# Kernel optimization log

Measured on AMD Instinct MI355X. Metric: run time of the kernel, lower is better.

Reference implementation:

```python
import jax, jax.numpy as jnp
import numpy as np
from jax import lax

KS = 3
PAD = 1
STRIDE = 1
N = KS * KS  # 9 sampling points
BN_EPS = 1e-5


def conv2d(x, w, stride=1, pad=0):
    return lax.conv_general_dilated(
        x, w, (stride, stride), [(pad, pad), (pad, pad)],
        dimension_numbers=('NCHW', 'OIHW', 'NCHW'))


def bn_inf(x, g, b, m, v):
    inv = g / jnp.sqrt(v + BN_EPS)
    return x * inv[None, :, None, None] + (b - m * inv)[None, :, None, None]


def gather_corners(x_flat, qx, qy, Wp):
    # x_flat: [B, C, Hp*Wp]; qx, qy: [B, H, W, N] int32
    B, C, _ = x_flat.shape
    idx = (qx * Wp + qy).reshape(B, 1, -1)
    out = jnp.take_along_axis(x_flat, jnp.broadcast_to(idx, (B, C, idx.shape[-1])), axis=-1)
    return out.reshape(B, C, *qx.shape[1:])  # [B, C, H, W, N]


def deform_conv_forward(x, w_conv1, g1, b1, m1, v1, w_dw, g2, b2, m2, v2,
                        w_conv2, g3, b3, m3, v3, w_out):
    B, C, H, W = x.shape
    identity = x

    # offset branch: Conv2d_BN(1x1) -> dwconv(3x3)+BN+ReLU -> Conv2d_BN(1x1)
    f = jax.nn.relu(bn_inf(conv2d(x, w_conv1), g1, b1, m1, v1))
    off = jax.nn.relu(bn_inf(conv2d(f, w_dw, pad=1), g2, b2, m2, v2))
    off = jax.nn.relu(bn_inf(conv2d(off, w_conv2), g3, b3, m3, v3))  # [B, 2N, H, W]
    off = off.transpose(0, 2, 3, 1)  # [B, H, W, 2N]

    # zero-pad input
    xp = jnp.pad(x, ((0, 0), (0, 0), (PAD, PAD), (PAD, PAD)))
    Hp, Wp = H + 2 * PAD, W + 2 * PAD

    # sampling locations p = p_0 + p_n + offset (x = row, y = col)
    rng = jnp.arange(-(KS - 1) // 2, (KS - 1) // 2 + 1, dtype=x.dtype)
    pnx, pny = jnp.meshgrid(rng, rng, indexing='ij')
    pnx, pny = pnx.ravel(), pny.ravel()  # [N]
    p0x = jnp.arange(1, H * STRIDE + 1, STRIDE, dtype=x.dtype)  # [H]
    p0y = jnp.arange(1, W * STRIDE + 1, STRIDE, dtype=x.dtype)  # [W]
    px = p0x[None, :, None, None] + pnx[None, None, None, :] + off[..., :N]  # [B,H,W,N]
    py = p0y[None, None, :, None] + pny[None, None, None, :] + off[..., N:]

    # integer corners (floor / floor+1, clamped) -- non-differentiable (detached in torch)
    flx = jnp.floor(lax.stop_gradient(px))
    fly = jnp.floor(lax.stop_gradient(py))
    qlt_x = jnp.clip(flx, 0, Hp - 1).astype(jnp.int32)
    qlt_y = jnp.clip(fly, 0, Wp - 1).astype(jnp.int32)
    qrb_x = jnp.clip(flx + 1, 0, Hp - 1).astype(jnp.int32)
    qrb_y = jnp.clip(fly + 1, 0, Wp - 1).astype(jnp.int32)

    # clamp continuous coords
    px = jnp.clip(px, 0, Hp - 1)
    py = jnp.clip(py, 0, Wp - 1)

    fx_lt = qlt_x.astype(px.dtype)
    fy_lt = qlt_y.astype(px.dtype)
    fx_rb = qrb_x.astype(px.dtype)
    fy_rb = qrb_y.astype(px.dtype)

    g_lt = (1 + (fx_lt - px)) * (1 + (fy_lt - py))
    g_rb = (1 - (fx_rb - px)) * (1 - (fy_rb - py))
    g_lb = (1 + (fx_lt - px)) * (1 - (fy_rb - py))
    g_rt = (1 - (fx_rb - px)) * (1 + (fy_lt - py))

    x_flat = xp.reshape(B, C, Hp * Wp)
    x_lt = gather_corners(x_flat, qlt_x, qlt_y, Wp)
    x_rb = gather_corners(x_flat, qrb_x, qrb_y, Wp)
    x_lb = gather_corners(x_flat, qlt_x, qrb_y, Wp)
    x_rt = gather_corners(x_flat, qrb_x, qlt_y, Wp)

    x_off = (g_lt[:, None] * x_lt + g_rb[:, None] * x_rb
             + g_lb[:, None] * x_lb + g_rt[:, None] * x_rt)  # [B,C,H,W,N]

    # reshape [B,C,H,W,ks,ks] -> [B,C,H*ks,W*ks] (matches torch _reshape_x_offset)
    x_off = x_off.reshape(B, C, H, W, KS, KS).transpose(0, 1, 2, 4, 3, 5)
    x_off = x_off.reshape(B, C, H * KS, W * KS)

    out = conv2d(x_off, w_out, stride=KS)  # [B, outc, H, W]
    return identity + out


def setup_inputs():
    key = jax.random.key(0)
    ks = jax.random.split(key, 8)
    B, C, H, W = 2, 64, 128, 128
    hid = int(C * 0.25)  # 16
    off_c = 2 * N  # 18
    x = jax.random.normal(ks[0], (B, C, H, W), jnp.float32)
    w_conv1 = jax.random.normal(ks[1], (hid, C, 1, 1), jnp.float32) * 0.1
    w_dw = jax.random.normal(ks[2], (off_c, hid, 3, 3), jnp.float32) * 0.05
    w_conv2 = jax.random.normal(ks[3], (off_c, off_c, 1, 1), jnp.float32) * 0.1
    w_out = jax.random.normal(ks[4], (C, C, KS, KS), jnp.float32) * 0.05

    def bn_params(k, c):
        k1, k2 = jax.random.split(k)
        return (1.0 + 0.1 * jax.random.normal(k1, (c,), jnp.float32),
                0.1 * jax.random.normal(k2, (c,), jnp.float32),
                jnp.zeros((c,), jnp.float32), jnp.ones((c,), jnp.float32))

    g1, b1, m1, v1 = bn_params(ks[5], hid)
    g2, b2, m2, v2 = bn_params(ks[6], off_c)
    g3, b3, m3, v3 = bn_params(ks[7], off_c)
    return dict(x=x, w_conv1=w_conv1, g1=g1, b1=b1, m1=m1, v1=v1,
                w_dw=w_dw, g2=g2, b2=b2, m2=m2, v2=v2,
                w_conv2=w_conv2, g3=g3, b3=b3, m3=m3, v3=v3, w_out=w_out)


def reference(x, w_conv1, g1, b1, m1, v1, w_dw, g2, b2, m2, v2,
              w_conv2, g3, b3, m3, v3, w_out):
    return deform_conv_forward(x, w_conv1, g1, b1, m1, v1, w_dw, g2, b2, m2, v2,
                               w_conv2, g3, b3, m3, v3, w_out)
```

## Files before the change

kernel.cpp:

```cpp
#include <hip/hip_runtime.h>

namespace {

constexpr int Hh = 128, Ww = 128, HW = 128 * 128;
constexpr int Cin = 64, HID = 16, OC = 18;

typedef __attribute__((ext_vector_type(8))) short short8;
typedef __attribute__((ext_vector_type(4))) float f32x4;

__device__ __forceinline__ unsigned short f2bf(float f) {
  unsigned u = __builtin_bit_cast(unsigned, f);
  unsigned rounded = u + 0x7fffu + ((u >> 16) & 1u);
  return (unsigned short)(rounded >> 16);
}
__device__ __forceinline__ float bf2f(unsigned short s) {
  unsigned u = ((unsigned)s) << 16;
  return __builtin_bit_cast(float, u);
}

__global__ __launch_bounds__(256) void k_pre(const float* __restrict__ x,
                                             unsigned short* __restrict__ xT,
                                             const float* __restrict__ w,
                                             unsigned short* __restrict__ wtb) {
  __shared__ float T[64][65];
  const int blk = blockIdx.x;
  const int t = threadIdx.x;
  if (blk >= 512) {
    const int i = (blk - 512) * 256 + t;
    const int oc = i / 576, r = i % 576;
    const int n = r >> 6, ic = r & 63;
    wtb[oc * 576 + r] = f2bf(w[oc * 576 + ic * 9 + n]);
    return;
  }
  const int b = blk >> 8;
  const int hw0 = (blk & 255) * 64;
  {
    const int p = t & 63, cg = t >> 6;
#pragma unroll
    for (int j = 0; j < 16; ++j) {
      const int c = cg * 16 + j;
      T[c][p] = x[(b * Cin + c) * HW + hw0 + p];
    }
  }
  __syncthreads();
  {
    const int c = t & 63, pg = t >> 6;
#pragma unroll
    for (int j = 0; j < 16; ++j) {
      const int p = pg * 16 + j;
      xT[((size_t)(b * HW + hw0 + p)) * 64 + c] = f2bf(T[c][p]);
    }
  }
}

__global__ __launch_bounds__(256) void k_off(
    const float* __restrict__ x, const float* __restrict__ w1,
    const float* __restrict__ g1, const float* __restrict__ b1,
    const float* __restrict__ m1, const float* __restrict__ v1,
    const float* __restrict__ wdw, const float* __restrict__ g2,
    const float* __restrict__ b2, const float* __restrict__ m2,
    const float* __restrict__ v2, const float* __restrict__ w2,
    const float* __restrict__ g3, const float* __restrict__ b3,
    const float* __restrict__ m3, const float* __restrict__ v3,
    float* __restrict__ offb) {
  __shared__ float fpart[2][HID][108];
  __shared__ float f[HID][108];
  __shared__ float off2[64][19];
  __shared__ float sA[16], bA[16], sB[18], bB[18], sC[18], bC[18];
  const int t = threadIdx.x;
  const int blk = blockIdx.x;
  const int b = blk >> 8;
  const int r0 = ((blk >> 3) & 31) * 4;
  const int c0 = (blk & 7) * 16;

  if (t >= 192 && t < 208) {
    int o = t - 192;
    float inv = g1[o] * rsqrtf(v1[o] + 1e-5f);
    sA[o] = inv; bA[o] = b1[o] - m1[o] * inv;
  } else if (t >= 208 && t < 226) {
    int o = t - 208;
    float inv = g2[o] * rsqrtf(v2[o] + 1e-5f);
    sB[o] = inv; bB[o] = b2[o] - m2[o] * inv;
  } else if (t >= 226 && t < 244) {
    int o = t - 226;
    float inv = g3[o] * rsqrtf(v3[o] + 1e-5f);
    sC[o] = inv; bC[o] = b3[o] - m3[o] * inv;
  }

  if (t < 216) {
    const int px = t % 108;
    const int cg = t / 108;
    const int hp = r0 + px / 18 - 1;
    const int wp = c0 + (px % 18) - 1;
    float acc[HID];
#pragma unroll
    for (int o = 0; o < HID; ++o) acc[o] = 0.f;
    if ((unsigned)hp < (unsigned)Hh && (unsigned)wp < (unsigned)Ww) {
      const float* xp = x + ((size_t)(b * Cin + cg * 32)) * HW + hp * Ww + wp;
      for (int c = 0; c < 32; ++c) {
        const float xv = xp[c * HW];
#pragma unroll
        for (int o = 0; o < HID; ++o)
          acc[o] = fmaf(w1[o * Cin + cg * 32 + c], xv, acc[o]);
      }
    }
#pragma unroll
    for (int o = 0; o < HID; ++o) fpart[cg][o][px] = acc[o];
  }
  __syncthreads();

  for (int idx = t; idx < 108 * HID; idx += 256) {
    const int px = idx % 108;
    const int o = idx / 108;
    const int hp = r0 + px / 18 - 1;
    const int wp = c0 + (px % 18) - 1;
    const float s = fpart[0][o][px] + fpart[1][o][px];
    const float y = fmaxf(fmaf(s, sA[o], bA[o]), 0.f);
    f[o][px] =
        ((unsigned)hp < (unsigned)Hh && (unsigned)wp < (unsigned)Ww) ? y : 0.f;
  }
  __syncthreads();

  if (t < 128) {
    const int ocg = t >> 6;
    const int px = t & 63;
    const int rr = px >> 4, cc = px & 15;
    float acc[9];
#pragma unroll
    for (int j = 0; j < 9; ++j) acc[j] = 0.f;
    for (int c = 0; c < HID; ++c) {
      float fv[9];
#pragma unroll
      for (int dh = 0; dh < 3; ++dh)
#pragma unroll
        for (int dw = 0; dw < 3; ++dw)
          fv[dh * 3 + dw] = f[c][(rr + dh) * 18 + cc + dw];
#pragma unroll
      for (int j = 0; j < 9; ++j) {
        const float* wj = wdw + (((ocg * 9 + j) * HID + c) * 9);
#pragma unroll
        for (int kk = 0; kk < 9; ++kk) acc[j] = fmaf(wj[kk], fv[kk], acc[j]);
      }
    }
#pragma unroll
    for (int j = 0; j < 9; ++j) {
      const int o = ocg * 9 + j;
      off2[px][o] = fmaxf(fmaf(acc[j], sB[o], bB[o]), 0.f);
    }
  }
  __syncthreads();

  if (t < 128) {
    const int ocg = t >> 6;
    const int px = t & 63;
    const int rr = px >> 4, cc = px & 15;
    float in[OC];
#pragma unroll
    for (int c = 0; c < OC; ++c) in[c] = off2[px][c];
    const int hw = (r0 + rr) * Ww + c0 + cc;
    float* dst = offb + ((size_t)(b * HW + hw)) * 18;
#pragma unroll
    for (int j = 0; j < 9; ++j) {
      const int o = ocg * 9 + j;
      float a = 0.f;
#pragma unroll
      for (int c = 0; c < OC; ++c) a = fmaf(w2[o * OC + c], in[c], a);
      dst[o] = fmaxf(fmaf(a, sC[o], bC[o]), 0.f);
    }
  }
}

__global__ __launch_bounds__(256) void k_main(
    const float* __restrict__ x, const unsigned short* __restrict__ xT,
    const float* __restrict__ offb, const unsigned short* __restrict__ wtb,
    float* __restrict__ out) {
  __shared__ unsigned short A[16][584];
  __shared__ float sg[16][9][4];
  __shared__ int si[16][9][4];
  const int blk = blockIdx.x;
  const int b = blk >> 10;
  const int t = threadIdx.x;
  const int hw0 = (blk & 1023) * 16;

  if (t < 144) {
    const int p = t / 9, n = t % 9;
    const int pix = blk * 16 + p;
    const int hw = pix & (HW - 1);
    const int h = hw >> 7, wc = hw & 127;
    const float offx = offb[pix * 18 + n];
    const float offy = offb[pix * 18 + 9 + n];
    const float px = (float)(h + (n / 3)) + offx;
    const float py = (float)(wc + (n % 3)) + offy;
    const float flx = floorf(px), fly = floorf(py);
    const float qltxf = fminf(fmaxf(flx, 0.f), 129.f);
    const float qltyf = fminf(fmaxf(fly, 0.f), 129.f);
    const float qrbxf = fminf(fmaxf(flx + 1.f, 0.f), 129.f);
    const float qrbyf = fminf(fmaxf(fly + 1.f, 0.f), 129.f);
    const float pxc = fminf(fmaxf(px, 0.f), 129.f);
    const float pyc = fminf(fmaxf(py, 0.f), 129.f);
    const float wx_lt = 1.f + (qltxf - pxc);
    const float wx_rb = 1.f - (qrbxf - pxc);
    const float wy_lt = 1.f + (qltyf - pyc);
    const float wy_rb = 1.f - (qrbyf - pyc);
    const int qltx = (int)qltxf, qlty = (int)qltyf;
    const int qrbx = (int)qrbxf, qrby = (int)qrbyf;
    const int cx[4] = {qltx, qrbx, qltx, qrbx};
    const int cy[4] = {qlty, qrby, qrby, qlty};
    const float gw[4] = {wx_lt * wy_lt, wx_rb * wy_rb, wx_lt * wy_rb,
                         wx_rb * wy_lt};
#pragma unroll
    for (int cc = 0; cc < 4; ++cc) {
      const bool valid =
          (cx[cc] >= 1) && (cx[cc] <= 128) && (cy[cc] >= 1) && (cy[cc] <= 128);
      si[p][n][cc] = valid ? ((cx[cc] - 1) * Ww + (cy[cc] - 1)) : 0;
      sg[p][n][cc] = valid ? gw[cc] : 0.f;
    }
  }
  __syncthreads();

  {
    const int p = t >> 4, ch4 = t & 15;
    const unsigned short* xb = xT + ((size_t)b * HW) * 64 + ch4 * 4;
#pragma unroll
    for (int n = 0; n < 9; ++n) {
      const ushort4 u0 = *(const ushort4*)(xb + (size_t)si[p][n][0] * 64);
      const ushort4 u1 = *(const ushort4*)(xb + (size_t)si[p][n][1] * 64);
      const ushort4 u2 = *(const ushort4*)(xb + (size_t)si[p][n][2] * 64);
      const ushort4 u3 = *(const ushort4*)(xb + (size_t)si[p][n][3] * 64);
      const float g0 = sg[p][n][0], g1 = sg[p][n][1], g2 = sg[p][n][2],
                  g3 = sg[p][n][3];
      float r0 = g0 * bf2f(u0.x);
      float r1 = g0 * bf2f(u0.y);
      float r2 = g0 * bf2f(u0.z);
      float r3 = g0 * bf2f(u0.w);
      r0 = fmaf(g1, bf2f(u1.x), r0); r1 = fmaf(g1, bf2f(u1.y), r1);
      r2 = fmaf(g1, bf2f(u1.z), r2); r3 = fmaf(g1, bf2f(u1.w), r3);
      r0 = fmaf(g2, bf2f(u2.x), r0); r1 = fmaf(g2, bf2f(u2.y), r1);
      r2 = fmaf(g2, bf2f(u2.z), r2); r3 = fmaf(g2, bf2f(u2.w), r3);
      r0 = fmaf(g3, bf2f(u3.x), r0); r1 = fmaf(g3, bf2f(u3.y), r1);
      r2 = fmaf(g3, bf2f(u3.z), r2); r3 = fmaf(g3, bf2f(u3.w), r3);
      ushort4 o;
      o.x = f2bf(r0); o.y = f2bf(r1); o.z = f2bf(r2); o.w = f2bf(r3);
      *(ushort4*)&A[p][n * 64 + ch4 * 4] = o;
    }
  }
  __syncthreads();

  {
    const int wv = t >> 6;
    const int lane = t & 63;
    const int l15 = lane & 15;
    const int quad = lane >> 4;
    const unsigned short* wrow = wtb + (size_t)(wv * 16 + l15) * 576 + quad * 8;
    const unsigned short* arow = &A[l15][quad * 8];
    f32x4 acc = {0.f, 0.f, 0.f, 0.f};
#pragma unroll
    for (int kb = 0; kb < 18; ++kb) {
      short8 af = *(const short8*)(wrow + kb * 32);
      short8 bf = *(const short8*)(arow + kb * 32);
      acc = __builtin_amdgcn_mfma_f32_16x16x32_bf16(af, bf, acc, 0, 0, 0);
    }
#pragma unroll
    for (int r = 0; r < 4; ++r) {
      const int oc = wv * 16 + quad * 4 + r;
      const size_t idx = ((size_t)(b * Cin + oc)) * HW + hw0 + l15;
      out[idx] = x[idx] + acc[r];
    }
  }
}

}

extern "C" void kernel_launch(void* const* d_in, const int* in_sizes, int n_in,
                              void* d_out, int out_size, void* d_ws,
                              size_t ws_size, hipStream_t stream) {
  const float* x = (const float*)d_in[0];
  const float* w1 = (const float*)d_in[1];
  const float* g1 = (const float*)d_in[2];
  const float* b1 = (const float*)d_in[3];
  const float* m1 = (const float*)d_in[4];
  const float* v1 = (const float*)d_in[5];
  const float* wdw = (const float*)d_in[6];
  const float* g2 = (const float*)d_in[7];
  const float* b2 = (const float*)d_in[8];
  const float* m2 = (const float*)d_in[9];
  const float* v2 = (const float*)d_in[10];
  const float* w2 = (const float*)d_in[11];
  const float* g3 = (const float*)d_in[12];
  const float* b3 = (const float*)d_in[13];
  const float* m3 = (const float*)d_in[14];
  const float* v3 = (const float*)d_in[15];
  const float* wout = (const float*)d_in[16];
  float* out = (float*)d_out;

  char* ws = (char*)d_ws;
  unsigned short* wtb = (unsigned short*)ws;
  unsigned short* xT = (unsigned short*)(ws + 81920);
  float* offb = (float*)(ws + 81920 + 4194304);

  k_pre<<<656, 256, 0, stream>>>(x, xT, wout, wtb);
  k_off<<<512, 256, 0, stream>>>(x, w1, g1, b1, m1, v1, wdw, g2, b2, m2, v2,
                                 w2, g3, b3, m3, v3, offb);
  k_main<<<2048, 256, 0, stream>>>(x, xT, offb, wtb, out);
}
```

Baseline: 153.2 us.

## Merge preprocessing and offset kernels into one launch with staged input halo

Combines the transpose/weight-conversion kernel and the offset-branch kernel into a single kernel, dispatching on block index, which removes one launch and lets the two independent jobs run concurrently. The offset branch now stages the 64-channel input halo tile into shared memory with a cooperative load before the 1x1 convolution, instead of each thread reading strided global memory. The union shared-memory buffer is larger (about 53 KB for every block), which may reduce occupancy for the transpose blocks.

```diff
diff --git a/kernel.cpp b/kernel.cpp
--- a/kernel.cpp
+++ b/kernel.cpp
@@ -18,60 +18,67 @@
   return __builtin_bit_cast(float, u);
 }
 
-__global__ __launch_bounds__(256) void k_pre(const float* __restrict__ x,
-                                             unsigned short* __restrict__ xT,
-                                             const float* __restrict__ w,
-                                             unsigned short* __restrict__ wtb) {
-  __shared__ float T[64][65];
+__global__ __launch_bounds__(256) void k_stage1(
+    const float* __restrict__ x, const float* __restrict__ wout,
+    const float* __restrict__ w1, const float* __restrict__ g1,
+    const float* __restrict__ b1, const float* __restrict__ m1,
+    const float* __restrict__ v1, const float* __restrict__ wdw,
+    const float* __restrict__ g2, const float* __restrict__ b2,
+    const float* __restrict__ m2, const float* __restrict__ v2,
+    const float* __restrict__ w2, const float* __restrict__ g3,
+    const float* __restrict__ b3, const float* __restrict__ m3,
+    const float* __restrict__ v3, unsigned short* __restrict__ xT,
+    unsigned short* __restrict__ wtb, float* __restrict__ offb) {
+  __shared__ __align__(16) char smem[53664];
   const int blk = blockIdx.x;
   const int t = threadIdx.x;
-  if (blk >= 512) {
+
+  if (blk < 512) {
+    float(*T)[65] = (float(*)[65])smem;
+    const int b = blk >> 8;
+    const int hw0 = (blk & 255) * 64;
+    {
+      const int p = t & 63, cg = t >> 6;
+#pragma unroll
+      for (int j = 0; j < 16; ++j) {
+        const int c = cg * 16 + j;
+        T[c][p] = x[(b * Cin + c) * HW + hw0 + p];
+      }
+    }
+    __syncthreads();
+    {
+      const int c = t & 63, pg = t >> 6;
+#pragma unroll
+      for (int j = 0; j < 16; ++j) {
+        const int p = pg * 16 + j;
+        xT[((size_t)(b * HW + hw0 + p)) * 64 + c] = f2bf(T[c][p]);
+      }
+    }
+    return;
+  }
+  if (blk < 656) {
     const int i = (blk - 512) * 256 + t;
     const int oc = i / 576, r = i % 576;
     const int n = r >> 6, ic = r & 63;
-    wtb[oc * 576 + r] = f2bf(w[oc * 576 + ic * 9 + n]);
+    wtb[oc * 576 + r] = f2bf(wout[oc * 576 + ic * 9 + n]);
     return;
   }
-  const int b = blk >> 8;
-  const int hw0 = (blk & 255) * 64;
-  {
-    const int p = t & 63, cg = t >> 6;
-#pragma unroll
-    for (int j = 0; j < 16; ++j) {
-      const int c = cg * 16 + j;
-      T[c][p] = x[(b * Cin + c) * HW + hw0 + p];
-    }
-  }
-  __syncthreads();
-  {
-    const int c = t & 63, pg = t >> 6;
-#pragma unroll
-    for (int j = 0; j < 16; ++j) {
-      const int p = pg * 16 + j;
-      xT[((size_t)(b * HW + hw0 + p)) * 64 + c] = f2bf(T[c][p]);
-    }
-  }
-}
-
-__global__ __launch_bounds__(256) void k_off(
-    const float* __restrict__ x, const float* __restrict__ w1,
-    const float* __restrict__ g1, const float* __restrict__ b1,
-    const float* __restrict__ m1, const float* __restrict__ v1,
-    const float* __restrict__ wdw, const float* __restrict__ g2,
-    const float* __restrict__ b2, const float* __restrict__ m2,
-    const float* __restrict__ v2, const float* __restrict__ w2,
-    const float* __restrict__ g3, const float* __restrict__ b3,
-    const float* __restrict__ m3, const float* __restrict__ v3,
-    float* __restrict__ offb) {
-  __shared__ float fpart[2][HID][108];
-  __shared__ float f[HID][108];
-  __shared__ float off2[64][19];
-  __shared__ float sA[16], bA[16], sB[18], bB[18], sC[18], bC[18];
-  const int t = threadIdx.x;
-  const int blk = blockIdx.x;
-  const int b = blk >> 8;
-  const int r0 = ((blk >> 3) & 31) * 4;
-  const int c0 = (blk & 7) * 16;
+
+  const int blk2 = blk - 656;
+  const int b = blk2 >> 8;
+  const int r0 = ((blk2 >> 3) & 31) * 4;
+  const int c0 = (blk2 & 7) * 16;
+  float* xh = (float*)smem;
+  float(*fpart)[HID][108] = (float(*)[HID][108])(smem + 27648);
+  float(*f)[108] = (float(*)[108])(smem + 41472);
+  float(*off2)[19] = (float(*)[19])(smem + 48384);
+  float* cst = (float*)(smem + 53248);
+  float* sA = cst;
+  float* bA = cst + 16;
+  float* sB = cst + 32;
+  float* bB = cst + 50;
+  float* sC = cst + 68;
+  float* bC = cst + 86;
 
   if (t >= 192 && t < 208) {
     int o = t - 192;
@@ -87,22 +94,31 @@
     sC[o] = inv; bC[o] = b3[o] - m3[o] * inv;
   }
 
+  {
+    const int base = b * Cin * HW;
+    for (int i = t; i < 64 * 108; i += 256) {
+      const int c = i / 108, px = i % 108;
+      const int hp = r0 + px / 18 - 1;
+      const int wp = c0 + (px % 18) - 1;
+      float v = 0.f;
+      if ((unsigned)hp < (unsigned)Hh && (unsigned)wp < (unsigned)Ww)
+        v = x[base + c * HW + hp * Ww + wp];
+      xh[c * 108 + px] = v;
+    }
+  }
+  __syncthreads();
+
   if (t < 216) {
     const int px = t % 108;
     const int cg = t / 108;
-    const int hp = r0 + px / 18 - 1;
-    const int wp = c0 + (px % 18) - 1;
     float acc[HID];
 #pragma unroll
     for (int o = 0; o < HID; ++o) acc[o] = 0.f;
-    if ((unsigned)hp < (unsigned)Hh && (unsigned)wp < (unsigned)Ww) {
-      const float* xp = x + ((size_t)(b * Cin + cg * 32)) * HW + hp * Ww + wp;
-      for (int c = 0; c < 32; ++c) {
-        const float xv = xp[c * HW];
-#pragma unroll
-        for (int o = 0; o < HID; ++o)
-          acc[o] = fmaf(w1[o * Cin + cg * 32 + c], xv, acc[o]);
-      }
+    for (int c = cg * 32; c < cg * 32 + 32; ++c) {
+      const float xv = xh[c * 108 + px];
+#pragma unroll
+      for (int o = 0; o < HID; ++o)
+        acc[o] = fmaf(w1[o * Cin + c], xv, acc[o]);
     }
 #pragma unroll
     for (int o = 0; o < HID; ++o) fpart[cg][o][px] = acc[o];
@@ -298,8 +314,8 @@
   unsigned short* xT = (unsigned short*)(ws + 81920);
   float* offb = (float*)(ws + 81920 + 4194304);
 
-  k_pre<<<656, 256, 0, stream>>>(x, xT, wout, wtb);
-  k_off<<<512, 256, 0, stream>>>(x, w1, g1, b1, m1, v1, wdw, g2, b2, m2, v2,
-                                 w2, g3, b3, m3, v3, offb);
+  k_stage1<<<1168, 256, 0, stream>>>(x, wout, w1, g1, b1, m1, v1, wdw, g2, b2,
+                                     m2, v2, w2, g3, b3, m3, v3, xT, wtb,
+                                     offb);
   k_main<<<2048, 256, 0, stream>>>(x, xT, offb, wtb, out);
 }
```

Measured after the change: 169.8 us. 10.8% more time.
